# Optimization experiments

Measured on AMD Instinct MI355X. Metric: run time of the kernel, lower is better.

Reference implementation:

```python
import jax, jax.numpy as jnp
import numpy as np

LARGE_CONSTANT = 1e9


def setup_inputs() -> dict:
    key = jax.random.key(0)
    ks = jax.random.split(key, 8)
    B, S, D, U = 8, 2048, 1024, 1024
    scale = 1.0 / np.sqrt(D)
    inputs_1 = jax.random.normal(ks[0], (B, S, D), dtype=jnp.float32)
    inputs_2 = jax.random.normal(ks[1], (B, S, D), dtype=jnp.float32)
    Wq = jax.random.normal(ks[2], (D, U), dtype=jnp.float32) * scale
    Wk = jax.random.normal(ks[3], (D, U), dtype=jnp.float32) * scale
    Wv = jax.random.normal(ks[4], (D, U), dtype=jnp.float32) * scale
    bq = jnp.zeros((U,), dtype=jnp.float32)
    bk = jnp.zeros((U,), dtype=jnp.float32)
    bv = jnp.zeros((U,), dtype=jnp.float32)
    # metric initialized as identity in the original; add small noise to exercise it
    metric = jnp.eye(U, dtype=jnp.float32) + 0.01 * jax.random.normal(ks[5], (U, U), dtype=jnp.float32)
    return {"inputs_1": inputs_1, "inputs_2": inputs_2, "Wq": Wq, "bq": bq,
            "Wk": Wk, "bk": bk, "Wv": Wv, "bv": bv, "metric": metric}


def reference(inputs_1, inputs_2, Wq, bq, Wk, bk, Wv, bv, metric):
    U = Wq.shape[1]
    scaling = jnp.sqrt(jnp.asarray(U, dtype=inputs_1.dtype))
    queries = inputs_1 @ Wq + bq            # [b, i, u]
    keys = inputs_2 @ Wk + bk               # [b, j, u]
    values = inputs_2 @ Wv + bv             # [b, j, u]
    queries = jnp.einsum('biu,uv->biv', queries, metric)  # learned-metric transform
    scores = jnp.einsum('biu,bju->bij', queries, keys) / scaling
    # causal mask: band_part(ones, -1, 0) is lower-triangular
    S = scores.shape[-1]
    causal = jnp.tril(jnp.ones((S, S), dtype=scores.dtype))
    scores = scores - LARGE_CONSTANT * (1.0 - causal)
    alpha = jax.nn.softmax(scores, axis=-1)
    return jnp.einsum('bij,bju->biu', alpha, values)
```

## Files before the change

kernel.cpp:

```cpp
#include <hip/hip_runtime.h>


#define Bq 8
#define Sq 2048
#define Dq 1024
#define Uq 1024

typedef __bf16 bf16;
typedef __bf16 bf16x8 __attribute__((ext_vector_type(8)));
typedef float f32x4 __attribute__((ext_vector_type(4)));
typedef unsigned short u16;
typedef unsigned int u32;

__device__ __forceinline__ u16 f2bf(float f) {
  u32 u = __builtin_bit_cast(u32, f);
  u32 r = u + 0x7fffu + ((u >> 16) & 1u);
  return (u16)(r >> 16);
}
__device__ __forceinline__ float bf2f(u32 h) {
  return __builtin_bit_cast(float, h << 16);
}

__device__ __forceinline__ void gl_lds16(const void* g, void* l) {
  __builtin_amdgcn_global_load_lds(
      (const __attribute__((address_space(1))) u32*)g,
      (__attribute__((address_space(3))) u32*)l, 16, 0, 0);
}


__global__ __launch_bounds__(256) void cvt_x(const float* __restrict__ x1,
                                             const float* __restrict__ x2,
                                             u16* __restrict__ o1,
                                             u16* __restrict__ o2, int n4) {
  int idx = blockIdx.x * 256 + threadIdx.x;
  if (idx >= n4) return;
  const float* in = blockIdx.y ? x2 : x1;
  u16* out = blockIdx.y ? o2 : o1;
  float4 v = ((const float4*)in)[idx];
  ushort4 o;
  o.x = f2bf(v.x); o.y = f2bf(v.y); o.z = f2bf(v.z); o.w = f2bf(v.w);
  ((ushort4*)out)[idx] = o;
}

__global__ __launch_bounds__(256) void cvt_bf16(const float* __restrict__ in,
                                                u16* __restrict__ out, int n4) {
  int idx = blockIdx.x * 256 + threadIdx.x;
  if (idx >= n4) return;
  float4 v = ((const float4*)in)[idx];
  ushort4 o;
  o.x = f2bf(v.x); o.y = f2bf(v.y); o.z = f2bf(v.z); o.w = f2bf(v.w);
  ((ushort4*)out)[idx] = o;
}

__global__ __launch_bounds__(256) void transpose_cvt3(
    const float* __restrict__ s0, u16* __restrict__ d0,
    const float* __restrict__ s1, u16* __restrict__ d1,
    const float* __restrict__ s2, u16* __restrict__ d2) {
  __shared__ float tile[32][33];
  const float* in = (blockIdx.z == 0) ? s0 : (blockIdx.z == 1) ? s1 : s2;
  u16* out = (blockIdx.z == 0) ? d0 : (blockIdx.z == 1) ? d1 : d2;
  const int N = 1024;
  int tx = threadIdx.x & 31, ty = threadIdx.x >> 5;
  int x0 = blockIdx.x * 32, y0 = blockIdx.y * 32;
#pragma unroll
  for (int r = 0; r < 32; r += 8)
    tile[ty + r][tx] = in[(size_t)(y0 + ty + r) * N + x0 + tx];
  __syncthreads();
#pragma unroll
  for (int r = 0; r < 32; r += 8)
    out[(size_t)(x0 + ty + r) * N + y0 + tx] = f2bf(tile[tx][ty + r]);
}

__global__ __launch_bounds__(256) void bqm_kernel(const float* __restrict__ bq,
                                                  const float* __restrict__ metric,
                                                  float* __restrict__ bqm) {
  int v = blockIdx.x * 256 + threadIdx.x;
  float s = 0.f;
  for (int u = 0; u < Uq; ++u) s += bq[u] * metric[(size_t)u * Uq + v];
  bqm[v] = s;
}

__global__ __launch_bounds__(256) void fill_zero(float4* __restrict__ p, int n4) {
  int i = blockIdx.x * 256 + threadIdx.x;
  if (i < n4) p[i] = float4{0.f, 0.f, 0.f, 0.f};
}

#define BM 128
#define BN 128
#define BK 32

template <int OUT_BF16, int BIAS>
__global__ __launch_bounds__(256) void gemm_tn(
    const bf16* __restrict__ A, const bf16* __restrict__ B, void* __restrict__ Cv,
    const float* __restrict__ bias, int lda, int ldb, int ldc,
    long long sA, long long sB, long long sC, int K,
    int causal_skip, int causal_klimit) {
  __shared__ __align__(16) bf16 lA[3][BM * BK];
  __shared__ __align__(16) bf16 lB[3][BN * BK];
  int bx = causal_klimit ? (gridDim.x - 1 - blockIdx.x) : blockIdx.x;
  int m0 = bx * BM, n0 = blockIdx.y * BN;
  if (causal_skip && n0 > m0 + BM - 1) return;
  long long b = blockIdx.z;
  A += b * sA;
  B += b * sB;
  int t = threadIdx.x;
  int w = t >> 6, l = t & 63;
  int wr = (w >> 1) * 64, wc = (w & 1) * 64;
  int Kend = causal_klimit ? min(K, m0 + BM) : K;
  int nk = Kend / BK;

  f32x4 acc[4][4] = {};
  int rowA = t >> 2, kc = (t & 3) * 8;
  int lm = l & 15, q = l >> 4;

  const bf16* gA = A + (long long)(m0 + rowA) * lda + kc;
  const bf16* gB = B + (long long)(n0 + rowA) * ldb + kc;
  long long a64 = (long long)64 * lda, b64 = (long long)64 * ldb;

  auto stage = [&](int kt, int buf) {
    int k0 = kt * BK;
    char* dA = (char*)lA[buf] + w * 1024;
    char* dB = (char*)lB[buf] + w * 1024;
    gl_lds16(gA + k0, dA);
    gl_lds16(gA + k0 + a64, dA + 4096);
    gl_lds16(gB + k0, dB);
    gl_lds16(gB + k0 + b64, dB + 4096);
  };

  stage(0, 0);
  stage(1, 1);
  int cur = 0;
  for (int kt = 0; kt < nk; ++kt) {
    if (kt + 2 < nk) {
      int pb = cur + 2;
      if (pb >= 3) pb -= 3;
      stage(kt + 2, pb);
      asm volatile("s_waitcnt vmcnt(8)\n\ts_barrier" ::: "memory");
    } else if (kt + 1 < nk) {
      asm volatile("s_waitcnt vmcnt(4)\n\ts_barrier" ::: "memory");
    } else {
      asm volatile("s_waitcnt vmcnt(0)\n\ts_barrier" ::: "memory");
    }
    bf16x8 af[4], bfr[4];
#pragma unroll
    for (int i = 0; i < 4; ++i)
      af[i] = *(const bf16x8*)&lA[cur][(wr + i * 16 + lm) * BK + q * 8];
#pragma unroll
    for (int i = 0; i < 4; ++i)
      bfr[i] = *(const bf16x8*)&lB[cur][(wc + i * 16 + lm) * BK + q * 8];
#pragma unroll
    for (int i = 0; i < 4; ++i)
#pragma unroll
      for (int j = 0; j < 4; ++j)
        acc[i][j] = __builtin_amdgcn_mfma_f32_16x16x32_bf16(af[i], bfr[j], acc[i][j], 0, 0, 0);
    asm volatile("s_barrier" ::: "memory");
    cur = (cur == 2) ? 0 : cur + 1;
  }

  char* Cb = (char*)Cv + (OUT_BF16 ? b * sC * 2 : b * sC * 4);
#pragma unroll
  for (int i = 0; i < 4; ++i) {
#pragma unroll
    for (int j = 0; j < 4; ++j) {
      int col = n0 + wc + j * 16 + lm;
      float bc = (BIAS == 1) ? bias[col] : 0.f;
#pragma unroll
      for (int r = 0; r < 4; ++r) {
        int row = m0 + wr + i * 16 + q * 4 + r;
        float v = acc[i][j][r] + bc;
        if (BIAS == 2) v += bias[row];
        size_t idx = (size_t)row * ldc + col;
        if (OUT_BF16)
          ((u16*)Cb)[idx] = f2bf(v);
        else
          ((float*)Cb)[idx] = v;
      }
    }
  }
}

__global__ __launch_bounds__(256) void softmax_causal(u16* __restrict__ sc) {
  __shared__ __align__(16) float sm[Sq];
  __shared__ float red[8];
  int gr = blockIdx.x;
  int i = gr & (Sq - 1);
  u16* rowp = sc + (size_t)gr * Sq;
  int t = threadIdx.x;
  uint4 pk = ((const uint4*)rowp)[t];
  float4 lo, hi;
  lo.x = bf2f(pk.x & 0xffffu); lo.y = bf2f(pk.x >> 16);
  lo.z = bf2f(pk.y & 0xffffu); lo.w = bf2f(pk.y >> 16);
  hi.x = bf2f(pk.z & 0xffffu); hi.y = bf2f(pk.z >> 16);
  hi.z = bf2f(pk.w & 0xffffu); hi.w = bf2f(pk.w >> 16);
  ((float4*)sm)[2 * t] = lo;
  ((float4*)sm)[2 * t + 1] = hi;
  __syncthreads();
  int nv = i + 1;
  const float scl = 0.03125f;
  float m = -1e30f;
  for (int j = t; j < nv; j += 256) m = fmaxf(m, sm[j]);
#pragma unroll
  for (int o = 32; o; o >>= 1) m = fmaxf(m, __shfl_xor(m, o));
  if ((t & 63) == 0) red[t >> 6] = m;
  __syncthreads();
  m = fmaxf(fmaxf(red[0], red[1]), fmaxf(red[2], red[3])) * scl;
  float sum = 0.f;
  for (int j = t; j < nv; j += 256) sum += __expf(sm[j] * scl - m);
#pragma unroll
  for (int o = 32; o; o >>= 1) sum += __shfl_xor(sum, o);
  if ((t & 63) == 0) red[4 + (t >> 6)] = sum;
  __syncthreads();
  float rinv = 1.0f / (red[4] + red[5] + red[6] + red[7]);
  int j0 = t * 8;
  u16 ov[8];
#pragma unroll
  for (int k = 0; k < 8; ++k)
    ov[k] = (j0 + k < nv) ? f2bf(__expf(sm[j0 + k] * scl - m) * rinv) : (u16)0;
  uint4 po;
  po.x = (u32)ov[0] | ((u32)ov[1] << 16);
  po.y = (u32)ov[2] | ((u32)ov[3] << 16);
  po.z = (u32)ov[4] | ((u32)ov[5] << 16);
  po.w = (u32)ov[6] | ((u32)ov[7] << 16);
  ((uint4*)rowp)[t] = po;
}


extern "C" void kernel_launch(void* const* d_in, const int* in_sizes, int n_in,
                              void* d_out, int out_size, void* d_ws, size_t ws_size,
                              hipStream_t stream) {
  const float* X1 = (const float*)d_in[0];
  const float* X2 = (const float*)d_in[1];
  const float* Wq = (const float*)d_in[2];
  const float* bq = (const float*)d_in[3];
  const float* Wk = (const float*)d_in[4];
  const float* bk = (const float*)d_in[5];
  const float* Wv = (const float*)d_in[6];
  const float* bv = (const float*)d_in[7];
  const float* metric = (const float*)d_in[8];
  float* out = (float*)d_out;

  const size_t XB = (size_t)Bq * Sq * Dq * 2;
  const size_t WB = (size_t)Dq * Uq * 2;
  const size_t NEED = 3 * XB + 5 * WB + 4096;

  if (ws_size < NEED) {
    fill_zero<<<(out_size / 4 + 255) / 256, 256, 0, stream>>>((float4*)d_out, out_size / 4);
    return;
  }

  char* ws = (char*)d_ws;
  bf16* X1b = (bf16*)(ws);
  bf16* X2b = (bf16*)(ws + XB);
  bf16* Vt = (bf16*)(ws + 2 * XB);
  bf16* WqB = (bf16*)(ws + 3 * XB);
  bf16* metT = (bf16*)(ws + 3 * XB + WB);
  bf16* WkT = (bf16*)(ws + 3 * XB + 2 * WB);
  bf16* WvT = (bf16*)(ws + 3 * XB + 3 * WB);
  bf16* WqmT = (bf16*)(ws + 3 * XB + 4 * WB);
  float* bqm = (float*)(ws + 3 * XB + 5 * WB);
  u16* Sc = (u16*)ws;
  bf16* Qb = (bf16*)d_out;
  bf16* Kb = (bf16*)d_out + (size_t)Bq * Sq * Uq;

  int nx4 = Bq * Sq * Dq / 4;
  cvt_x<<<dim3((nx4 + 255) / 256, 2), 256, 0, stream>>>(X1, X2, (u16*)X1b, (u16*)X2b, nx4);
  cvt_bf16<<<(Dq * Uq / 4 + 255) / 256, 256, 0, stream>>>(Wq, (u16*)WqB, Dq * Uq / 4);
  transpose_cvt3<<<dim3(32, 32, 3), 256, 0, stream>>>(
      metric, (u16*)metT, Wk, (u16*)WkT, Wv, (u16*)WvT);
  bqm_kernel<<<Uq / 256, 256, 0, stream>>>(bq, metric, bqm);

  gemm_tn<1, 0><<<dim3(Uq / BM, Dq / BN, 1), 256, 0, stream>>>(
      metT, WqB, WqmT, nullptr, Uq, Uq, Dq, 0, 0, 0, Uq, 0, 0);

  const int MQ = Bq * Sq;
  gemm_tn<1, 1><<<dim3(MQ / BM, Uq / BN, 1), 256, 0, stream>>>(
      X1b, WqmT, Qb, bqm, Dq, Dq, Uq, 0, 0, 0, Dq, 0, 0);
  gemm_tn<1, 1><<<dim3(MQ / BM, Uq / BN, 1), 256, 0, stream>>>(
      X2b, WkT, Kb, bk, Dq, Dq, Uq, 0, 0, 0, Dq, 0, 0);
  gemm_tn<1, 2><<<dim3(Uq / BM, Sq / BN, Bq), 256, 0, stream>>>(
      WvT, X2b, Vt, bv, Dq, Dq, Sq, 0, (long long)Sq * Dq, (long long)Uq * Sq, Dq, 0, 0);

  gemm_tn<1, 0><<<dim3(Sq / BM, Sq / BN, Bq), 256, 0, stream>>>(
      Qb, Kb, Sc, nullptr, Uq, Uq, Sq, (long long)Sq * Uq, (long long)Sq * Uq,
      (long long)Sq * Sq, Uq, 1, 0);

  softmax_causal<<<Bq * Sq, 256, 0, stream>>>(Sc);

  gemm_tn<0, 0><<<dim3(Sq / BM, Uq / BN, Bq), 256, 0, stream>>>(
      (const bf16*)Sc, Vt, out, nullptr, Sq, Sq, Uq, (long long)Sq * Sq,
      (long long)Uq * Sq, (long long)Sq * Uq, Sq, 0, 1);

  (void)in_sizes; (void)n_in; (void)ws_size;
}
```

Before: 596.0 us.

## Add 256x256-tile 512-thread GEMM with 4-stage LDS pipeline; trim softmax traffic

```diff
diff --git a/kernel.cpp b/kernel.cpp
--- a/kernel.cpp
+++ b/kernel.cpp
@@ -179,6 +179,108 @@
   }
 }
 
+
+template <int OUT_BF16, int BIAS>
+__global__ __launch_bounds__(512, 2) void gemm_tn256(
+    const bf16* __restrict__ A, const bf16* __restrict__ B, void* __restrict__ Cv,
+    const float* __restrict__ bias, int lda, int ldb, int ldc,
+    long long sA, long long sB, long long sC, int K,
+    int causal_skip, int causal_klimit) {
+  __shared__ __align__(16) bf16 lA[4][256 * 32];
+  __shared__ __align__(16) bf16 lB[4][256 * 32];
+  int bx = causal_klimit ? (gridDim.x - 1 - blockIdx.x) : blockIdx.x;
+  int m0 = bx * 256, n0 = blockIdx.y * 256;
+  if (causal_skip && n0 > m0 + 255) return;
+  long long b = blockIdx.z;
+  A += b * sA;
+  B += b * sB;
+  int t = threadIdx.x;
+  int w = t >> 6, l = t & 63;
+  int wr = w >> 2, wc = w & 3;
+  int lm = l & 15, q = l >> 4;
+  int cq = q ^ ((lm >> 1) & 3);
+
+  int Kend = causal_klimit ? min(K, m0 + 256) : K;
+  int NP = Kend >> 5;
+
+  int r0 = t >> 2;
+  int c0 = t & 3;
+  int q0 = c0 ^ ((r0 >> 1) & 3);
+  const bf16* gA0 = A + (long long)(m0 + r0) * lda + q0 * 8;
+  const bf16* gA1 = gA0 + (long long)128 * lda;
+  const bf16* gB0 = B + (long long)(n0 + r0) * ldb + q0 * 8;
+  const bf16* gB1 = gB0 + (long long)128 * ldb;
+  char* dA = (char*)&lA[0][0] + w * 1024;
+  char* dB = (char*)&lB[0][0] + w * 1024;
+
+  auto stage = [&](int ph) {
+    int reg_ = ph & 3;
+    int k0 = ph << 5;
+    char* da = dA + reg_ * 16384;
+    char* db = dB + reg_ * 16384;
+    gl_lds16(gA0 + k0, da);
+    gl_lds16(gA1 + k0, da + 8192);
+    gl_lds16(gB0 + k0, db);
+    gl_lds16(gB1 + k0, db + 8192);
+  };
+
+  stage(0); stage(1); stage(2); stage(3);
+
+  f32x4 acc[8][4] = {};
+  const bf16* pAl = &lA[0][0] + (wr * 128 + lm) * 32 + cq * 8;
+  const bf16* pBl = &lB[0][0] + (wc * 64 + lm) * 32 + cq * 8;
+
+  for (int p = 0; p < NP; ++p) {
+    if (p + 3 < NP)
+      asm volatile("s_waitcnt vmcnt(12)\n\ts_barrier" ::: "memory");
+    else if (p + 2 < NP)
+      asm volatile("s_waitcnt vmcnt(8)\n\ts_barrier" ::: "memory");
+    else if (p + 1 < NP)
+      asm volatile("s_waitcnt vmcnt(4)\n\ts_barrier" ::: "memory");
+    else
+      asm volatile("s_waitcnt vmcnt(0)\n\ts_barrier" ::: "memory");
+
+    int reg_ = p & 3;
+    const bf16* pa = pAl + reg_ * 8192;
+    const bf16* pb = pBl + reg_ * 8192;
+    bf16x8 af[8], bfr[4];
+#pragma unroll
+    for (int j = 0; j < 4; ++j) bfr[j] = *(const bf16x8*)(pb + j * 512);
+#pragma unroll
+    for (int i = 0; i < 8; ++i) af[i] = *(const bf16x8*)(pa + i * 512);
+    __builtin_amdgcn_s_setprio(1);
+#pragma unroll
+    for (int i = 0; i < 8; ++i)
+#pragma unroll
+      for (int j = 0; j < 4; ++j)
+        acc[i][j] = __builtin_amdgcn_mfma_f32_16x16x32_bf16(af[i], bfr[j], acc[i][j], 0, 0, 0);
+    __builtin_amdgcn_s_setprio(0);
+    asm volatile("s_barrier" ::: "memory");
+    if (p + 4 < NP) stage(p + 4);
+  }
+
+  char* Cb = (char*)Cv + (OUT_BF16 ? b * sC * 2 : b * sC * 4);
+#pragma unroll
+  for (int i = 0; i < 8; ++i) {
+#pragma unroll
+    for (int j = 0; j < 4; ++j) {
+      int col = n0 + wc * 64 + j * 16 + lm;
+      float bc = (BIAS == 1) ? bias[col] : 0.f;
+#pragma unroll
+      for (int r = 0; r < 4; ++r) {
+        int row = m0 + wr * 128 + i * 16 + q * 4 + r;
+        float v = acc[i][j][r] + bc;
+        if (BIAS == 2) v += bias[row];
+        size_t idxc = (size_t)row * ldc + col;
+        if (OUT_BF16)
+          ((u16*)Cb)[idxc] = f2bf(v);
+        else
+          ((float*)Cb)[idxc] = v;
+      }
+    }
+  }
+}
+
 __global__ __launch_bounds__(256) void softmax_causal(u16* __restrict__ sc) {
   __shared__ __align__(16) float sm[Sq];
   __shared__ float red[8];
@@ -186,16 +288,20 @@
   int i = gr & (Sq - 1);
   u16* rowp = sc + (size_t)gr * Sq;
   int t = threadIdx.x;
-  uint4 pk = ((const uint4*)rowp)[t];
-  float4 lo, hi;
-  lo.x = bf2f(pk.x & 0xffffu); lo.y = bf2f(pk.x >> 16);
-  lo.z = bf2f(pk.y & 0xffffu); lo.w = bf2f(pk.y >> 16);
-  hi.x = bf2f(pk.z & 0xffffu); hi.y = bf2f(pk.z >> 16);
-  hi.z = bf2f(pk.w & 0xffffu); hi.w = bf2f(pk.w >> 16);
-  ((float4*)sm)[2 * t] = lo;
-  ((float4*)sm)[2 * t + 1] = hi;
+  int nv = i + 1;
+  int wlim = (i & ~255) + 256;
+  int j0 = t * 8;
+  if (j0 < nv) {
+    uint4 pk = ((const uint4*)rowp)[t];
+    float4 lo, hi;
+    lo.x = bf2f(pk.x & 0xffffu); lo.y = bf2f(pk.x >> 16);
+    lo.z = bf2f(pk.y & 0xffffu); lo.w = bf2f(pk.y >> 16);
+    hi.x = bf2f(pk.z & 0xffffu); hi.y = bf2f(pk.z >> 16);
+    hi.z = bf2f(pk.w & 0xffffu); hi.w = bf2f(pk.w >> 16);
+    ((float4*)sm)[2 * t] = lo;
+    ((float4*)sm)[2 * t + 1] = hi;
+  }
   __syncthreads();
-  int nv = i + 1;
   const float scl = 0.03125f;
   float m = -1e30f;
   for (int j = t; j < nv; j += 256) m = fmaxf(m, sm[j]);
@@ -211,17 +317,18 @@
   if ((t & 63) == 0) red[4 + (t >> 6)] = sum;
   __syncthreads();
   float rinv = 1.0f / (red[4] + red[5] + red[6] + red[7]);
-  int j0 = t * 8;
-  u16 ov[8];
-#pragma unroll
-  for (int k = 0; k < 8; ++k)
-    ov[k] = (j0 + k < nv) ? f2bf(__expf(sm[j0 + k] * scl - m) * rinv) : (u16)0;
-  uint4 po;
-  po.x = (u32)ov[0] | ((u32)ov[1] << 16);
-  po.y = (u32)ov[2] | ((u32)ov[3] << 16);
-  po.z = (u32)ov[4] | ((u32)ov[5] << 16);
-  po.w = (u32)ov[6] | ((u32)ov[7] << 16);
-  ((uint4*)rowp)[t] = po;
+  if (j0 < wlim) {
+    u16 ov[8];
+#pragma unroll
+    for (int k = 0; k < 8; ++k)
+      ov[k] = (j0 + k < nv) ? f2bf(__expf(sm[j0 + k] * scl - m) * rinv) : (u16)0;
+    uint4 po;
+    po.x = (u32)ov[0] | ((u32)ov[1] << 16);
+    po.y = (u32)ov[2] | ((u32)ov[3] << 16);
+    po.z = (u32)ov[4] | ((u32)ov[5] << 16);
+    po.w = (u32)ov[6] | ((u32)ov[7] << 16);
+    ((uint4*)rowp)[t] = po;
+  }
 }
 
 
@@ -273,20 +380,20 @@
       metT, WqB, WqmT, nullptr, Uq, Uq, Dq, 0, 0, 0, Uq, 0, 0);
 
   const int MQ = Bq * Sq;
-  gemm_tn<1, 1><<<dim3(MQ / BM, Uq / BN, 1), 256, 0, stream>>>(
+  gemm_tn256<1, 1><<<dim3(MQ / 256, Uq / 256, 1), 512, 0, stream>>>(
       X1b, WqmT, Qb, bqm, Dq, Dq, Uq, 0, 0, 0, Dq, 0, 0);
-  gemm_tn<1, 1><<<dim3(MQ / BM, Uq / BN, 1), 256, 0, stream>>>(
+  gemm_tn256<1, 1><<<dim3(MQ / 256, Uq / 256, 1), 512, 0, stream>>>(
       X2b, WkT, Kb, bk, Dq, Dq, Uq, 0, 0, 0, Dq, 0, 0);
-  gemm_tn<1, 2><<<dim3(Uq / BM, Sq / BN, Bq), 256, 0, stream>>>(
+  gemm_tn256<1, 2><<<dim3(Uq / 256, Sq / 256, Bq), 512, 0, stream>>>(
       WvT, X2b, Vt, bv, Dq, Dq, Sq, 0, (long long)Sq * Dq, (long long)Uq * Sq, Dq, 0, 0);
 
-  gemm_tn<1, 0><<<dim3(Sq / BM, Sq / BN, Bq), 256, 0, stream>>>(
+  gemm_tn256<1, 0><<<dim3(Sq / 256, Sq / 256, Bq), 512, 0, stream>>>(
       Qb, Kb, Sc, nullptr, Uq, Uq, Sq, (long long)Sq * Uq, (long long)Sq * Uq,
       (long long)Sq * Sq, Uq, 1, 0);
 
   softmax_causal<<<Bq * Sq, 256, 0, stream>>>(Sc);
 
-  gemm_tn<0, 0><<<dim3(Sq / BM, Uq / BN, Bq), 256, 0, stream>>>(
+  gemm_tn256<0, 0><<<dim3(Sq / 256, Uq / 256, Bq), 512, 0, stream>>>(
       (const bf16*)Sc, Vt, out, nullptr, Sq, Sq, Uq, (long long)Sq * Sq,
       (long long)Uq * Sq, (long long)Sq * Uq, Sq, 0, 1);
 
```

Measured after the change: 568.6 us. -4.6%, faster.
